# Kernel tuning notes

Hardware: AMD Instinct MI355X
Metric: run time of the kernel (lower is better)

The kernel has to match this reference:

```python
import jax, jax.numpy as jnp
import numpy as np

B, S, F, E, K = 4, 1024, 1024, 8, 2
H = 4 * F  # expert hidden dim, hard-coded as features*4 in the module


def setup_inputs() -> dict:
    key = jax.random.key(0)
    ks = jax.random.split(key, 7)
    def xavier(k, shape):
        fan_in, fan_out = shape[-2], shape[-1]
        scale = jnp.sqrt(6.0 / (fan_in + fan_out))
        return jax.random.uniform(k, shape, jnp.float32, -scale, scale)
    return {
        "x": jax.random.normal(ks[0], (B, S, F), jnp.float32),
        "Wg": xavier(ks[1], (F, E)),
        "bg": jnp.zeros((E,), jnp.float32),
        "W1": xavier(ks[2], (E, F, H)),
        "b1": jnp.zeros((E, H), jnp.float32),
        "W2": xavier(ks[3], (E, H, F)),
        "b2": jnp.zeros((E, F), jnp.float32),
    }


def reference(x, Wg, bg, W1, b1, W2, b2):
    # Gating: softmax over experts, keep top-k, renormalize.
    gate_probs = jax.nn.softmax(x @ Wg + bg, axis=-1)              # (b,s,E)
    k = K
    _, top_idx = jax.lax.top_k(gate_probs, k)                       # (b,s,k)
    expert_mask = jax.nn.one_hot(top_idx, gate_probs.shape[-1],
                                 dtype=gate_probs.dtype).sum(-2)    # (b,s,E)
    selected = gate_probs * expert_mask
    selected = selected / (selected.sum(-1, keepdims=True) + 1e-8)
    # Dense all-expert 2-layer MLP (gelu, tanh approximation as in flax nn.gelu).
    h = jax.nn.gelu(jnp.einsum('bsf,efh->bseh', x, W1) + b1)        # (b,s,E,H)
    expert_out = jnp.einsum('bseh,ehf->bsef', h, W2) + b2[None, None]  # (b,s,E,F)
    # Weighted combine over experts with renormalized top-k gates.
    return jnp.einsum('bsef,bse->bsf', expert_out, selected)
```

## Files before the change

kernel.cpp:

```cpp
#include <hip/hip_runtime.h>
#include <hip/hip_bf16.h>

constexpr int Ff = 1024;
constexpr int Ee = 8;
constexpr int Hh = 4096;
constexpr int T  = 4096;
constexpr int MB = 80;

typedef short     bf16x8 __attribute__((ext_vector_type(8)));
typedef float     f32x4  __attribute__((ext_vector_type(4)));
typedef unsigned short u16x8 __attribute__((ext_vector_type(8)));

__device__ __forceinline__ float gelu_fast(float v) {
  const float c2 = 2.0f * 0.7978845608028654f;
  float z2 = c2 * (v + 0.044715f * v * v * v);
  return v / (1.0f + __expf(-z2));
}

__device__ __forceinline__ unsigned short bf16bits(float f) {
  __hip_bfloat16 h = __float2bfloat16(f);
  return *reinterpret_cast<unsigned short*>(&h);
}

__device__ __forceinline__ void gl_lds16(const void* g, void* l) {
  __builtin_amdgcn_global_load_lds(
      (const __attribute__((address_space(1))) unsigned int*)g,
      (__attribute__((address_space(3))) unsigned int*)l, 16, 0, 0);
}

__global__ __launch_bounds__(256) void gating_kernel(
    const float* __restrict__ x, const float* __restrict__ Wg,
    const float* __restrict__ bg, int* __restrict__ cnt,
    int* __restrict__ list, float* __restrict__ wlist) {
  const int wave = threadIdx.x >> 6;
  const int lane = threadIdx.x & 63;
  const int t = blockIdx.x * 4 + wave;
  float acc[Ee] = {0.f,0.f,0.f,0.f,0.f,0.f,0.f,0.f};
  const float* xrow = x + (size_t)t * Ff;
  for (int f0 = 0; f0 < Ff; f0 += 64) {
    float xv = xrow[f0 + lane];
    const float* wrow = Wg + (size_t)(f0 + lane) * Ee;
    float4 w0 = *reinterpret_cast<const float4*>(wrow);
    float4 w1 = *reinterpret_cast<const float4*>(wrow + 4);
    acc[0] += xv * w0.x; acc[1] += xv * w0.y;
    acc[2] += xv * w0.z; acc[3] += xv * w0.w;
    acc[4] += xv * w1.x; acc[5] += xv * w1.y;
    acc[6] += xv * w1.z; acc[7] += xv * w1.w;
  }
#pragma unroll
  for (int e = 0; e < Ee; ++e) {
#pragma unroll
    for (int off = 32; off; off >>= 1) acc[e] += __shfl_xor(acc[e], off);
  }
  if (lane == 0) {
    float l[Ee], m = -1e30f;
#pragma unroll
    for (int e = 0; e < Ee; ++e) { l[e] = acc[e] + bg[e]; m = fmaxf(m, l[e]); }
    float p[Ee], Z = 0.f;
#pragma unroll
    for (int e = 0; e < Ee; ++e) { p[e] = expf(l[e] - m); Z += p[e]; }
#pragma unroll
    for (int e = 0; e < Ee; ++e) p[e] /= Z;
    int i1 = 0; float p1 = p[0];
#pragma unroll
    for (int e = 1; e < Ee; ++e) if (p[e] > p1) { p1 = p[e]; i1 = e; }
    int i2 = -1; float p2 = -1e30f;
#pragma unroll
    for (int e = 0; e < Ee; ++e) if (e != i1 && p[e] > p2) { p2 = p[e]; i2 = e; }
    float denom = p1 + p2 + 1e-8f;
    int pos = atomicAdd(&cnt[i1], 1);
    list[i1 * T + pos] = t; wlist[i1 * T + pos] = p1 / denom;
    pos = atomicAdd(&cnt[i2], 1);
    list[i2 * T + pos] = t; wlist[i2 * T + pos] = p2 / denom;
  }
}

__global__ void prefix_kernel(const int* __restrict__ cnt, int* __restrict__ offs) {
  if (threadIdx.x == 0) {
    int s = 0;
    for (int e = 0; e < Ee; ++e) { offs[e] = s; s += (cnt[e] + 127) & ~127; }
    offs[Ee] = s;
  }
}

__global__ __launch_bounds__(256) void pack_w_kernel(
    const float* __restrict__ src, unsigned short* __restrict__ dst,
    int sN, size_t s_estride, size_t d_estride, int KT) {
  const int e  = blockIdx.z;
  const int nb = blockIdx.x;
  const int kt = blockIdx.y;
  __shared__ float Ts[128][33];
  const int t = threadIdx.x;
  const float* sb = src + (size_t)e * s_estride + (size_t)(kt * 32) * sN + nb * 128;
  {
    const int row = t >> 5;
    const int cc  = (t & 31) * 4;
#pragma unroll
    for (int i = 0; i < 4; ++i) {
      float4 v = *reinterpret_cast<const float4*>(sb + (size_t)(row + 8 * i) * sN + cc);
      Ts[cc + 0][row + 8 * i] = v.x;
      Ts[cc + 1][row + 8 * i] = v.y;
      Ts[cc + 2][row + 8 * i] = v.z;
      Ts[cc + 3][row + 8 * i] = v.w;
    }
  }
  __syncthreads();
  unsigned short* db = dst + (size_t)e * d_estride + ((size_t)nb * KT + kt) * 4096;
#pragma unroll
  for (int j = 0; j < 2; ++j) {
    const int idx = t + 256 * j;
    const int col = idx & 127, kb = idx >> 7;
    u16x8 o;
#pragma unroll
    for (int q = 0; q < 8; ++q) o[q] = bf16bits(Ts[col][kb * 8 + q]);
    *reinterpret_cast<u16x8*>(db + kb * 1024 + col * 8) = o;
  }
}

__global__ __launch_bounds__(256) void pack_x_kernel(
    const float* __restrict__ x, const int* __restrict__ cnt,
    const int* __restrict__ offs, const int* __restrict__ list,
    unsigned short* __restrict__ xg) {
  const int kt = blockIdx.x;
  const int mb = blockIdx.y;
  const int t = threadIdx.x;
  const int m0g = mb * 128;
  int e = 0;
#pragma unroll
  for (int i = 1; i < Ee; ++i) e += (m0g >= offs[i]) ? 1 : 0;
  const int ce = cnt[e];
  const int row = t >> 1, half = t & 1;
  const int mloc = m0g - offs[e] + row;
  const bool valid = (mloc >= 0) && (mloc < ce);
  const int token = valid ? list[e * T + mloc] : 0;
  const float* sp = x + (size_t)token * Ff + kt * 32 + half * 16;
  u16x8 o0, o1;
#pragma unroll
  for (int i = 0; i < 2; ++i) {
    float4 v = valid ? *reinterpret_cast<const float4*>(sp + i * 4)
                     : make_float4(0.f, 0.f, 0.f, 0.f);
    o0[i * 4 + 0] = bf16bits(v.x); o0[i * 4 + 1] = bf16bits(v.y);
    o0[i * 4 + 2] = bf16bits(v.z); o0[i * 4 + 3] = bf16bits(v.w);
  }
#pragma unroll
  for (int i = 2; i < 4; ++i) {
    float4 v = valid ? *reinterpret_cast<const float4*>(sp + i * 4)
                     : make_float4(0.f, 0.f, 0.f, 0.f);
    o1[(i - 2) * 4 + 0] = bf16bits(v.x); o1[(i - 2) * 4 + 1] = bf16bits(v.y);
    o1[(i - 2) * 4 + 2] = bf16bits(v.z); o1[(i - 2) * 4 + 3] = bf16bits(v.w);
  }
  unsigned short* db = xg + ((size_t)mb * (Ff / 32) + kt) * 4096 + row * 8;
  *reinterpret_cast<u16x8*>(db + (half * 2 + 0) * 1024) = o0;
  *reinterpret_cast<u16x8*>(db + (half * 2 + 1) * 1024) = o1;
}

__global__ __launch_bounds__(256, 3) void gemm1_mfma(
    const unsigned short* __restrict__ xg, const unsigned short* __restrict__ W1P,
    const float* __restrict__ b1, const int* __restrict__ cnt,
    const int* __restrict__ offs, unsigned short* __restrict__ hp, int Hc, int c) {
  const int nxg = Hc >> 7;
  const int nwg = nxg * MB;
  const int raw = blockIdx.x;
  int bid = (raw & 7) * (nwg >> 3) + (raw >> 3);
  const int bw = (nxg >= 4) ? 4 : nxg;
  const int band = bid / (MB * bw);
  const int r2 = bid % (MB * bw);
  const int by = r2 / bw;
  const int bx = band * bw + (r2 % bw);

  const int m0g = by * 128;
  int e = 0;
#pragma unroll
  for (int i = 1; i < Ee; ++i) e += (m0g >= offs[i]) ? 1 : 0;
  const int ce = cnt[e];
  const int mloc = m0g - offs[e];
  if (mloc >= ce) return;
  const int n0 = bx * 128;

  __shared__ __align__(16) unsigned short AsF[3 * 4096];
  __shared__ __align__(16) unsigned short BsF[3 * 4096];

  const int tid = threadIdx.x;
  const int w = tid >> 6, lane = tid & 63;
  const int g = lane >> 4, r16 = lane & 15;
  const int wr = w >> 1, wc = w & 1;

  constexpr int NT = Ff / 32;
  const unsigned short* aU = xg  + (size_t)by * NT * 4096;
  const unsigned short* bU = W1P + (size_t)(e * nxg + bx) * NT * 4096;

  f32x4 acc[4][4] = {};
  auto STAGE = [&](int buf, int kt) {
    const unsigned short* aS = aU + (size_t)kt * 4096 + w * 1024 + lane * 8;
    const unsigned short* bS = bU + (size_t)kt * 4096 + w * 1024 + lane * 8;
    unsigned short* aD = AsF + buf * 4096 + w * 1024;
    unsigned short* bD = BsF + buf * 4096 + w * 1024;
    gl_lds16(aS,       aD);
    gl_lds16(aS + 512, aD + 512);
    gl_lds16(bS,       bD);
    gl_lds16(bS + 512, bD + 512);
  };
  STAGE(0, 0); STAGE(1, 1);
  int cur = 0;
#pragma unroll 1
  for (int t = 0; t < NT; ++t) {
    if (t + 1 < NT) asm volatile("s_waitcnt vmcnt(4)" ::: "memory");
    else            asm volatile("s_waitcnt vmcnt(0)" ::: "memory");
    __builtin_amdgcn_s_barrier();
    asm volatile("" ::: "memory");
    if (t + 2 < NT) STAGE((t + 2) % 3, t + 2);
    bf16x8 af[4], bfr[4];
#pragma unroll
    for (int i = 0; i < 4; ++i) {
      af[i]  = *reinterpret_cast<const bf16x8*>(
          AsF + cur * 4096 + g * 1024 + (wr * 64 + i * 16 + r16) * 8);
      bfr[i] = *reinterpret_cast<const bf16x8*>(
          BsF + cur * 4096 + g * 1024 + (wc * 64 + i * 16 + r16) * 8);
    }
    asm volatile("s_waitcnt lgkmcnt(0)" ::: "memory");
    __builtin_amdgcn_sched_barrier(0);
    __builtin_amdgcn_s_setprio(1);
#pragma unroll
    for (int mi = 0; mi < 4; ++mi)
#pragma unroll
      for (int ni = 0; ni < 4; ++ni)
        acc[mi][ni] = __builtin_amdgcn_mfma_f32_16x16x32_bf16(
            af[mi], bfr[ni], acc[mi][ni], 0, 0, 0);
    __builtin_amdgcn_s_setprio(0);
    asm volatile("" ::: "memory");
    cur = (cur == 2) ? 0 : cur + 1;
  }
  const int KT2 = Hc >> 5;
  unsigned short* hb = hp + (size_t)by * KT2 * 4096;
#pragma unroll
  for (int ni = 0; ni < 4; ++ni) {
    const int col = n0 + wc * 64 + ni * 16 + r16;
    const float bias = b1[(size_t)e * Hh + (size_t)c * Hc + col];
    unsigned short* hcol = hb + ((size_t)(col >> 5) * 4 + ((col >> 3) & 3)) * 1024 + (col & 7);
#pragma unroll
    for (int mi = 0; mi < 4; ++mi)
#pragma unroll
      for (int r = 0; r < 4; ++r) {
        const int row = wr * 64 + mi * 16 + g * 4 + r;
        if (mloc + row < ce)
          hcol[row * 8] = bf16bits(gelu_fast(acc[mi][ni][r] + bias));
      }
  }
}

__global__ __launch_bounds__(256, 3) void gemm2_mfma(
    const unsigned short* __restrict__ hp, const unsigned short* __restrict__ W2P,
    const float* __restrict__ b2, const int* __restrict__ cnt,
    const int* __restrict__ offs, const int* __restrict__ list,
    const float* __restrict__ wlist, float* __restrict__ out,
    int Hc, int kLen, int ksplit, int biasC) {
  constexpr int nxg = Ff >> 7;
  const int nwg = nxg * MB * ksplit;
  const int raw = blockIdx.x;
  int bid = (raw & 7) * (nwg >> 3) + (raw >> 3);
  const int bx = bid % nxg;
  const int rest = bid / nxg;
  const int by = rest % MB;
  const int bz = rest / MB;

  const int m0g = by * 128;
  int e = 0;
#pragma unroll
  for (int i = 1; i < Ee; ++i) e += (m0g >= offs[i]) ? 1 : 0;
  const int ce = cnt[e];
  const int mloc = m0g - offs[e];
  if (mloc >= ce) return;
  const int n0 = bx * 128;

  __shared__ __align__(16) unsigned short AsF[3 * 4096];
  __shared__ __align__(16) unsigned short BsF[3 * 4096];

  const int tid = threadIdx.x;
  const int w = tid >> 6, lane = tid & 63;
  const int g = lane >> 4, r16 = lane & 15;
  const int wr = w >> 1, wc = w & 1;

  const int KT2 = Hc >> 5;
  const int ktOff = (bz * kLen) >> 5;
  const int NT = kLen >> 5;
  const unsigned short* aU = hp  + ((size_t)by * KT2 + ktOff) * 4096;
  const unsigned short* bU = W2P + ((size_t)(e * nxg + bx) * KT2 + ktOff) * 4096;

  f32x4 acc[4][4] = {};
  auto STAGE = [&](int buf, int kt) {
    const unsigned short* aS = aU + (size_t)kt * 4096 + w * 1024 + lane * 8;
    const unsigned short* bS = bU + (size_t)kt * 4096 + w * 1024 + lane * 8;
    unsigned short* aD = AsF + buf * 4096 + w * 1024;
    unsigned short* bD = BsF + buf * 4096 + w * 1024;
    gl_lds16(aS,       aD);
    gl_lds16(aS + 512, aD + 512);
    gl_lds16(bS,       bD);
    gl_lds16(bS + 512, bD + 512);
  };
  STAGE(0, 0);
  if (NT > 1) STAGE(1, 1);
  int cur = 0;
#pragma unroll 1
  for (int t = 0; t < NT; ++t) {
    if (t + 1 < NT) asm volatile("s_waitcnt vmcnt(4)" ::: "memory");
    else            asm volatile("s_waitcnt vmcnt(0)" ::: "memory");
    __builtin_amdgcn_s_barrier();
    asm volatile("" ::: "memory");
    if (t + 2 < NT) STAGE((t + 2) % 3, t + 2);
    bf16x8 af[4], bfr[4];
#pragma unroll
    for (int i = 0; i < 4; ++i) {
      af[i]  = *reinterpret_cast<const bf16x8*>(
          AsF + cur * 4096 + g * 1024 + (wr * 64 + i * 16 + r16) * 8);
      bfr[i] = *reinterpret_cast<const bf16x8*>(
          BsF + cur * 4096 + g * 1024 + (wc * 64 + i * 16 + r16) * 8);
    }
    asm volatile("s_waitcnt lgkmcnt(0)" ::: "memory");
    __builtin_amdgcn_sched_barrier(0);
    __builtin_amdgcn_s_setprio(1);
#pragma unroll
    for (int mi = 0; mi < 4; ++mi)
#pragma unroll
      for (int ni = 0; ni < 4; ++ni)
        acc[mi][ni] = __builtin_amdgcn_mfma_f32_16x16x32_bf16(
            af[mi], bfr[ni], acc[mi][ni], 0, 0, 0);
    __builtin_amdgcn_s_setprio(0);
    asm volatile("" ::: "memory");
    cur = (cur == 2) ? 0 : cur + 1;
  }
  const bool addBias = (biasC != 0) && (bz == 0);
#pragma unroll
  for (int mi = 0; mi < 4; ++mi)
#pragma unroll
    for (int r = 0; r < 4; ++r) {
      const int row = wr * 64 + mi * 16 + g * 4 + r;
      if (mloc + row >= ce) continue;
      const int token = list[e * T + mloc + row];
      const float wgt = wlist[e * T + mloc + row];
      float* op = out + (size_t)token * Ff;
#pragma unroll
      for (int ni = 0; ni < 4; ++ni) {
        const int col = n0 + wc * 64 + ni * 16 + r16;
        float v = acc[mi][ni][r];
        if (addBias) v += b2[(size_t)e * Ff + col];
        atomicAdd(&op[col], wgt * v);
      }
    }
}

extern "C" void kernel_launch(void* const* d_in, const int* in_sizes, int n_in,
                              void* d_out, int out_size, void* d_ws, size_t ws_size,
                              hipStream_t stream) {
  const float* x  = (const float*)d_in[0];
  const float* Wg = (const float*)d_in[1];
  const float* bg = (const float*)d_in[2];
  const float* W1 = (const float*)d_in[3];
  const float* b1 = (const float*)d_in[4];
  const float* W2 = (const float*)d_in[5];
  const float* b2 = (const float*)d_in[6];
  float* out = (float*)d_out;

  const size_t fixed = 1024 + 2 * (size_t)T * Ee * 4 + (size_t)MB * 128 * Ff * 2;
  int Hc = 4096;
  while (Hc > 256 && fixed + (size_t)Hc * 53248 > ws_size) Hc >>= 1;
  const int nchunk = Hh / Hc;
  const int ksplit = 2;
  const int kLen = Hc / ksplit;

  char* p = (char*)d_ws;
  int*   cnt   = (int*)p;            p += 512;
  int*   offs  = (int*)p;            p += 512;
  int*   list  = (int*)p;            p += (size_t)T * Ee * 4;
  float* wlist = (float*)p;          p += (size_t)T * Ee * 4;
  unsigned short* xg  = (unsigned short*)p;  p += (size_t)MB * 128 * Ff * 2;
  unsigned short* W1P = (unsigned short*)p;  p += (size_t)Ee * Hc * Ff * 2;
  unsigned short* W2P = (unsigned short*)p;  p += (size_t)Ee * Ff * Hc * 2;
  unsigned short* hp  = (unsigned short*)p;

  hipMemsetAsync(d_out, 0, (size_t)out_size * sizeof(float), stream);
  hipMemsetAsync(cnt, 0, 64, stream);

  gating_kernel<<<T / 4, 256, 0, stream>>>(x, Wg, bg, cnt, list, wlist);
  prefix_kernel<<<1, 64, 0, stream>>>(cnt, offs);
  pack_x_kernel<<<dim3(Ff / 32, MB), 256, 0, stream>>>(x, cnt, offs, list, xg);

  for (int c = 0; c < nchunk; ++c) {
    pack_w_kernel<<<dim3(Hc / 128, Ff / 32, Ee), 256, 0, stream>>>(
        W1 + (size_t)c * Hc, W1P, Hh, (size_t)Ff * Hh, (size_t)Hc * Ff, Ff / 32);
    pack_w_kernel<<<dim3(Ff / 128, Hc / 32, Ee), 256, 0, stream>>>(
        W2 + (size_t)c * Hc * Ff, W2P, Ff, (size_t)Hh * Ff, (size_t)Ff * Hc, Hc / 32);
    gemm1_mfma<<<(Hc / 128) * MB, 256, 0, stream>>>(
        xg, W1P, b1, cnt, offs, hp, Hc, c);
    gemm2_mfma<<<(Ff / 128) * MB * ksplit, 256, 0, stream>>>(
        hp, W2P, b2, cnt, offs, list, wlist, out, Hc, kLen, ksplit,
        c == nchunk - 1 ? 1 : 0);
  }
}
```

Measured before the change: 501.1 us.

## Enlarge MoE GEMM tiles to 256x128 with 512 threads and K=64 stages

```diff
diff --git a/kernel.cpp b/kernel.cpp
--- a/kernel.cpp
+++ b/kernel.cpp
@@ -5,7 +5,8 @@
 constexpr int Ee = 8;
 constexpr int Hh = 4096;
 constexpr int T  = 4096;
-constexpr int MB = 80;
+constexpr int MB128 = 80;
+constexpr int MBLK  = 40;
 
 typedef short     bf16x8 __attribute__((ext_vector_type(8)));
 typedef float     f32x4  __attribute__((ext_vector_type(4)));
@@ -78,7 +79,7 @@
 __global__ void prefix_kernel(const int* __restrict__ cnt, int* __restrict__ offs) {
   if (threadIdx.x == 0) {
     int s = 0;
-    for (int e = 0; e < Ee; ++e) { offs[e] = s; s += (cnt[e] + 127) & ~127; }
+    for (int e = 0; e < Ee; ++e) { offs[e] = s; s += (cnt[e] + 255) & ~255; }
     offs[Ee] = s;
   }
 }
@@ -154,21 +155,87 @@
   *reinterpret_cast<u16x8*>(db + (half * 2 + 1) * 1024) = o1;
 }
 
-__global__ __launch_bounds__(256, 3) void gemm1_mfma(
+
+#define GEMM_CORE_LOOP(aU0, aU1, bU)                                                    \
+  f32x4 acc[4][4] = {};                                                                 \
+  auto LOAD1 = [&](int l, int tb, int tt) {                                             \
+    const int rgn = l >> 4, j = l & 15;                                                 \
+    const int s2 = j >> 3, kb = (j >> 1) & 3, hh = j & 1;                               \
+    const int off = (s2 * 4 + kb) * 1024 + hh * 512;                                    \
+    unsigned short* dst = (rgn < 2) ? (SMEM + tb * 24576 + rgn * 8192 + off)            \
+                                    : (SMEM + tb * 24576 + 16384 + off);                \
+    const unsigned short* srcb = (rgn == 0) ? (aU0) : (rgn == 1) ? (aU1) : (bU);        \
+    const unsigned short* src = srcb + (size_t)(2 * tt + s2) * 4096 + kb * 1024         \
+                                + hh * 512 + lane * 8;                                  \
+    gl_lds16(src, dst);                                                                 \
+  };                                                                                    \
+  {                                                                                     \
+    for (int i = 0; i < 6; ++i) LOAD1(6 * w + i, 0, 0);                                 \
+    if (NT > 1) { for (int i = 0; i < 6; ++i) LOAD1(6 * w + i, 1, 1); }                 \
+    asm volatile("s_waitcnt vmcnt(6)" ::: "memory");                                    \
+    __builtin_amdgcn_s_barrier();                                                       \
+  }                                                                                     \
+  _Pragma("unroll 1")                                                                   \
+  for (int t = 0; t < NT; ++t) {                                                        \
+    const int cb = t % 3;                                                               \
+    const int tb = (t + 2) % 3;                                                         \
+    const bool st = (t + 2) < NT;                                                       \
+    _Pragma("unroll")                                                                   \
+    for (int ph = 0; ph < 2; ++ph) {                                                    \
+      bf16x8 a2[2][2], b4[4][2];                                                        \
+      _Pragma("unroll")                                                                 \
+      for (int f = 0; f < 2; ++f)                                                       \
+        _Pragma("unroll")                                                               \
+        for (int s = 0; s < 2; ++s) {                                                   \
+          const int row = (wm & 1) * 64 + (ph * 2 + f) * 16 + r16;                      \
+          a2[f][s] = *reinterpret_cast<const bf16x8*>(                                  \
+              SMEM + cb * 24576 + (wm >> 1) * 8192 + (s * 4 + g) * 1024 + row * 8);     \
+        }                                                                               \
+      _Pragma("unroll")                                                                 \
+      for (int nf = 0; nf < 4; ++nf)                                                    \
+        _Pragma("unroll")                                                               \
+        for (int s = 0; s < 2; ++s)                                                     \
+          b4[nf][s] = *reinterpret_cast<const bf16x8*>(                                 \
+              SMEM + cb * 24576 + 16384 + (s * 4 + g) * 1024 +                          \
+              (wn * 64 + nf * 16 + r16) * 8);                                           \
+      if (st) {                                                                         \
+        LOAD1(6 * w + 3 * ph + 0, tb, t + 2);                                           \
+        LOAD1(6 * w + 3 * ph + 1, tb, t + 2);                                           \
+        LOAD1(6 * w + 3 * ph + 2, tb, t + 2);                                           \
+      }                                                                                 \
+      if (ph == 1) {                                                                    \
+        if (st) asm volatile("s_waitcnt vmcnt(6)" ::: "memory");                        \
+        else    asm volatile("s_waitcnt vmcnt(0)" ::: "memory");                        \
+      }                                                                                 \
+      __builtin_amdgcn_s_barrier();                                                     \
+      asm volatile("s_waitcnt lgkmcnt(0)" ::: "memory");                                \
+      __builtin_amdgcn_sched_barrier(0);                                                \
+      __builtin_amdgcn_s_setprio(1);                                                    \
+      _Pragma("unroll")                                                                 \
+      for (int f = 0; f < 2; ++f)                                                       \
+        _Pragma("unroll")                                                               \
+        for (int nf = 0; nf < 4; ++nf)                                                  \
+          _Pragma("unroll")                                                             \
+          for (int s = 0; s < 2; ++s)                                                   \
+            acc[ph * 2 + f][nf] = __builtin_amdgcn_mfma_f32_16x16x32_bf16(              \
+                a2[f][s], b4[nf][s], acc[ph * 2 + f][nf], 0, 0, 0);                     \
+      __builtin_amdgcn_s_setprio(0);                                                    \
+      asm volatile("" ::: "memory");                                                    \
+      __builtin_amdgcn_s_barrier();                                                     \
+    }                                                                                   \
+  }
+
+__global__ __launch_bounds__(512, 2) void gemm1_mfma(
     const unsigned short* __restrict__ xg, const unsigned short* __restrict__ W1P,
     const float* __restrict__ b1, const int* __restrict__ cnt,
     const int* __restrict__ offs, unsigned short* __restrict__ hp, int Hc, int c) {
   const int nxg = Hc >> 7;
-  const int nwg = nxg * MB;
+  const int nwg = nxg * MBLK;
   const int raw = blockIdx.x;
   int bid = (raw & 7) * (nwg >> 3) + (raw >> 3);
-  const int bw = (nxg >= 4) ? 4 : nxg;
-  const int band = bid / (MB * bw);
-  const int r2 = bid % (MB * bw);
-  const int by = r2 / bw;
-  const int bx = band * bw + (r2 % bw);
-
-  const int m0g = by * 128;
+  const int by = bid % MBLK;
+  const int bx = bid / MBLK;
+  const int m0g = by * 256;
   int e = 0;
 #pragma unroll
   for (int i = 1; i < Ee; ++i) e += (m0g >= offs[i]) ? 1 : 0;
@@ -177,93 +244,65 @@
   if (mloc >= ce) return;
   const int n0 = bx * 128;
 
-  __shared__ __align__(16) unsigned short AsF[3 * 4096];
-  __shared__ __align__(16) unsigned short BsF[3 * 4096];
+  __shared__ __align__(16) unsigned short SMEM[73728];
 
   const int tid = threadIdx.x;
   const int w = tid >> 6, lane = tid & 63;
   const int g = lane >> 4, r16 = lane & 15;
-  const int wr = w >> 1, wc = w & 1;
-
-  constexpr int NT = Ff / 32;
-  const unsigned short* aU = xg  + (size_t)by * NT * 4096;
-  const unsigned short* bU = W1P + (size_t)(e * nxg + bx) * NT * 4096;
-
-  f32x4 acc[4][4] = {};
-  auto STAGE = [&](int buf, int kt) {
-    const unsigned short* aS = aU + (size_t)kt * 4096 + w * 1024 + lane * 8;
-    const unsigned short* bS = bU + (size_t)kt * 4096 + w * 1024 + lane * 8;
-    unsigned short* aD = AsF + buf * 4096 + w * 1024;
-    unsigned short* bD = BsF + buf * 4096 + w * 1024;
-    gl_lds16(aS,       aD);
-    gl_lds16(aS + 512, aD + 512);
-    gl_lds16(bS,       bD);
-    gl_lds16(bS + 512, bD + 512);
-  };
-  STAGE(0, 0); STAGE(1, 1);
-  int cur = 0;
-#pragma unroll 1
-  for (int t = 0; t < NT; ++t) {
-    if (t + 1 < NT) asm volatile("s_waitcnt vmcnt(4)" ::: "memory");
-    else            asm volatile("s_waitcnt vmcnt(0)" ::: "memory");
-    __builtin_amdgcn_s_barrier();
-    asm volatile("" ::: "memory");
-    if (t + 2 < NT) STAGE((t + 2) % 3, t + 2);
-    bf16x8 af[4], bfr[4];
-#pragma unroll
-    for (int i = 0; i < 4; ++i) {
-      af[i]  = *reinterpret_cast<const bf16x8*>(
-          AsF + cur * 4096 + g * 1024 + (wr * 64 + i * 16 + r16) * 8);
-      bfr[i] = *reinterpret_cast<const bf16x8*>(
-          BsF + cur * 4096 + g * 1024 + (wc * 64 + i * 16 + r16) * 8);
-    }
-    asm volatile("s_waitcnt lgkmcnt(0)" ::: "memory");
-    __builtin_amdgcn_sched_barrier(0);
-    __builtin_amdgcn_s_setprio(1);
-#pragma unroll
-    for (int mi = 0; mi < 4; ++mi)
-#pragma unroll
-      for (int ni = 0; ni < 4; ++ni)
-        acc[mi][ni] = __builtin_amdgcn_mfma_f32_16x16x32_bf16(
-            af[mi], bfr[ni], acc[mi][ni], 0, 0, 0);
-    __builtin_amdgcn_s_setprio(0);
-    asm volatile("" ::: "memory");
-    cur = (cur == 2) ? 0 : cur + 1;
-  }
+  const int wm = w >> 1, wn = w & 1;
+
+  constexpr int NT = Ff / 64;
+  const unsigned short* aU0 = xg + (size_t)(2 * by + 0) * (Ff / 32) * 4096;
+  const unsigned short* aU1 = xg + (size_t)(2 * by + 1) * (Ff / 32) * 4096;
+  const unsigned short* bU  = W1P + (size_t)(e * nxg + bx) * (Ff / 32) * 4096;
+
+  GEMM_CORE_LOOP(aU0, aU1, bU)
+
+  __builtin_amdgcn_s_barrier();
+  unsigned short* Ls = SMEM;
+#pragma unroll
+  for (int nf = 0; nf < 4; ++nf) {
+    const int col = wn * 64 + nf * 16 + r16;
+    const float bias = b1[(size_t)e * Hh + (size_t)c * Hc + n0 + col];
+#pragma unroll
+    for (int mf = 0; mf < 4; ++mf)
+#pragma unroll
+      for (int r = 0; r < 4; ++r) {
+        const int row = wm * 64 + mf * 16 + g * 4 + r;
+        Ls[row * 136 + col] = bf16bits(gelu_fast(acc[mf][nf][r] + bias));
+      }
+  }
+  __builtin_amdgcn_s_barrier();
   const int KT2 = Hc >> 5;
-  unsigned short* hb = hp + (size_t)by * KT2 * 4096;
-#pragma unroll
-  for (int ni = 0; ni < 4; ++ni) {
-    const int col = n0 + wc * 64 + ni * 16 + r16;
-    const float bias = b1[(size_t)e * Hh + (size_t)c * Hc + col];
-    unsigned short* hcol = hb + ((size_t)(col >> 5) * 4 + ((col >> 3) & 3)) * 1024 + (col & 7);
-#pragma unroll
-    for (int mi = 0; mi < 4; ++mi)
-#pragma unroll
-      for (int r = 0; r < 4; ++r) {
-        const int row = wr * 64 + mi * 16 + g * 4 + r;
-        if (mloc + row < ce)
-          hcol[row * 8] = bf16bits(gelu_fast(acc[mi][ni][r] + bias));
-      }
-  }
-}
-
-__global__ __launch_bounds__(256, 3) void gemm2_mfma(
+#pragma unroll
+  for (int p = 0; p < 8; ++p) {
+    const int u = p * 512 + tid;
+    const int oct = u >> 8;
+    const int row = u & 255;
+    const int lc = oct * 8;
+    unsigned short* dst = hp +
+        ((size_t)(2 * by + (row >> 7)) * KT2 + ((n0 + lc) >> 5)) * 4096 +
+        ((lc >> 3) & 3) * 1024 + (row & 127) * 8;
+    *reinterpret_cast<u16x8*>(dst) = *reinterpret_cast<const u16x8*>(&Ls[row * 136 + lc]);
+  }
+}
+
+__global__ __launch_bounds__(512, 2) void gemm2_mfma(
     const unsigned short* __restrict__ hp, const unsigned short* __restrict__ W2P,
     const float* __restrict__ b2, const int* __restrict__ cnt,
     const int* __restrict__ offs, const int* __restrict__ list,
     const float* __restrict__ wlist, float* __restrict__ out,
     int Hc, int kLen, int ksplit, int biasC) {
   constexpr int nxg = Ff >> 7;
-  const int nwg = nxg * MB * ksplit;
+  const int nwg = nxg * MBLK * ksplit;
   const int raw = blockIdx.x;
   int bid = (raw & 7) * (nwg >> 3) + (raw >> 3);
   const int bx = bid % nxg;
   const int rest = bid / nxg;
-  const int by = rest % MB;
-  const int bz = rest / MB;
-
-  const int m0g = by * 128;
+  const int by = rest % MBLK;
+  const int bz = rest / MBLK;
+
+  const int m0g = by * 256;
   int e = 0;
 #pragma unroll
   for (int i = 1; i < Ee; ++i) e += (m0g >= offs[i]) ? 1 : 0;
@@ -272,76 +311,36 @@
   if (mloc >= ce) return;
   const int n0 = bx * 128;
 
-  __shared__ __align__(16) unsigned short AsF[3 * 4096];
-  __shared__ __align__(16) unsigned short BsF[3 * 4096];
+  __shared__ __align__(16) unsigned short SMEM[73728];
 
   const int tid = threadIdx.x;
   const int w = tid >> 6, lane = tid & 63;
   const int g = lane >> 4, r16 = lane & 15;
-  const int wr = w >> 1, wc = w & 1;
+  const int wm = w >> 1, wn = w & 1;
 
   const int KT2 = Hc >> 5;
   const int ktOff = (bz * kLen) >> 5;
-  const int NT = kLen >> 5;
-  const unsigned short* aU = hp  + ((size_t)by * KT2 + ktOff) * 4096;
-  const unsigned short* bU = W2P + ((size_t)(e * nxg + bx) * KT2 + ktOff) * 4096;
-
-  f32x4 acc[4][4] = {};
-  auto STAGE = [&](int buf, int kt) {
-    const unsigned short* aS = aU + (size_t)kt * 4096 + w * 1024 + lane * 8;
-    const unsigned short* bS = bU + (size_t)kt * 4096 + w * 1024 + lane * 8;
-    unsigned short* aD = AsF + buf * 4096 + w * 1024;
-    unsigned short* bD = BsF + buf * 4096 + w * 1024;
-    gl_lds16(aS,       aD);
-    gl_lds16(aS + 512, aD + 512);
-    gl_lds16(bS,       bD);
-    gl_lds16(bS + 512, bD + 512);
-  };
-  STAGE(0, 0);
-  if (NT > 1) STAGE(1, 1);
-  int cur = 0;
-#pragma unroll 1
-  for (int t = 0; t < NT; ++t) {
-    if (t + 1 < NT) asm volatile("s_waitcnt vmcnt(4)" ::: "memory");
-    else            asm volatile("s_waitcnt vmcnt(0)" ::: "memory");
-    __builtin_amdgcn_s_barrier();
-    asm volatile("" ::: "memory");
-    if (t + 2 < NT) STAGE((t + 2) % 3, t + 2);
-    bf16x8 af[4], bfr[4];
-#pragma unroll
-    for (int i = 0; i < 4; ++i) {
-      af[i]  = *reinterpret_cast<const bf16x8*>(
-          AsF + cur * 4096 + g * 1024 + (wr * 64 + i * 16 + r16) * 8);
-      bfr[i] = *reinterpret_cast<const bf16x8*>(
-          BsF + cur * 4096 + g * 1024 + (wc * 64 + i * 16 + r16) * 8);
-    }
-    asm volatile("s_waitcnt lgkmcnt(0)" ::: "memory");
-    __builtin_amdgcn_sched_barrier(0);
-    __builtin_amdgcn_s_setprio(1);
-#pragma unroll
-    for (int mi = 0; mi < 4; ++mi)
-#pragma unroll
-      for (int ni = 0; ni < 4; ++ni)
-        acc[mi][ni] = __builtin_amdgcn_mfma_f32_16x16x32_bf16(
-            af[mi], bfr[ni], acc[mi][ni], 0, 0, 0);
-    __builtin_amdgcn_s_setprio(0);
-    asm volatile("" ::: "memory");
-    cur = (cur == 2) ? 0 : cur + 1;
-  }
+  const int NT = kLen >> 6;
+  const unsigned short* aU0 = hp + ((size_t)(2 * by + 0) * KT2 + ktOff) * 4096;
+  const unsigned short* aU1 = hp + ((size_t)(2 * by + 1) * KT2 + ktOff) * 4096;
+  const unsigned short* bU  = W2P + ((size_t)(e * nxg + bx) * KT2 + ktOff) * 4096;
+
+  GEMM_CORE_LOOP(aU0, aU1, bU)
+
   const bool addBias = (biasC != 0) && (bz == 0);
 #pragma unroll
-  for (int mi = 0; mi < 4; ++mi)
+  for (int mf = 0; mf < 4; ++mf)
 #pragma unroll
     for (int r = 0; r < 4; ++r) {
-      const int row = wr * 64 + mi * 16 + g * 4 + r;
+      const int row = wm * 64 + mf * 16 + g * 4 + r;
       if (mloc + row >= ce) continue;
       const int token = list[e * T + mloc + row];
       const float wgt = wlist[e * T + mloc + row];
       float* op = out + (size_t)token * Ff;
 #pragma unroll
-      for (int ni = 0; ni < 4; ++ni) {
-        const int col = n0 + wc * 64 + ni * 16 + r16;
-        float v = acc[mi][ni][r];
+      for (int nf = 0; nf < 4; ++nf) {
+        const int col = n0 + wn * 64 + nf * 16 + r16;
+        float v = acc[mf][nf][r];
         if (addBias) v += b2[(size_t)e * Ff + col];
         atomicAdd(&op[col], wgt * v);
       }
@@ -360,7 +359,7 @@
   const float* b2 = (const float*)d_in[6];
   float* out = (float*)d_out;
 
-  const size_t fixed = 1024 + 2 * (size_t)T * Ee * 4 + (size_t)MB * 128 * Ff * 2;
+  const size_t fixed = 1024 + 2 * (size_t)T * Ee * 4 + (size_t)MB128 * 128 * Ff * 2;
   int Hc = 4096;
   while (Hc > 256 && fixed + (size_t)Hc * 53248 > ws_size) Hc >>= 1;
   const int nchunk = Hh / Hc;
@@ -372,7 +371,7 @@
   int*   offs  = (int*)p;            p += 512;
   int*   list  = (int*)p;            p += (size_t)T * Ee * 4;
   float* wlist = (float*)p;          p += (size_t)T * Ee * 4;
-  unsigned short* xg  = (unsigned short*)p;  p += (size_t)MB * 128 * Ff * 2;
+  unsigned short* xg  = (unsigned short*)p;  p += (size_t)MB128 * 128 * Ff * 2;
   unsigned short* W1P = (unsigned short*)p;  p += (size_t)Ee * Hc * Ff * 2;
   unsigned short* W2P = (unsigned short*)p;  p += (size_t)Ee * Ff * Hc * 2;
   unsigned short* hp  = (unsigned short*)p;
@@ -382,16 +381,16 @@
 
   gating_kernel<<<T / 4, 256, 0, stream>>>(x, Wg, bg, cnt, list, wlist);
   prefix_kernel<<<1, 64, 0, stream>>>(cnt, offs);
-  pack_x_kernel<<<dim3(Ff / 32, MB), 256, 0, stream>>>(x, cnt, offs, list, xg);
+  pack_x_kernel<<<dim3(Ff / 32, MB128), 256, 0, stream>>>(x, cnt, offs, list, xg);
 
   for (int c = 0; c < nchunk; ++c) {
     pack_w_kernel<<<dim3(Hc / 128, Ff / 32, Ee), 256, 0, stream>>>(
         W1 + (size_t)c * Hc, W1P, Hh, (size_t)Ff * Hh, (size_t)Hc * Ff, Ff / 32);
     pack_w_kernel<<<dim3(Ff / 128, Hc / 32, Ee), 256, 0, stream>>>(
         W2 + (size_t)c * Hc * Ff, W2P, Ff, (size_t)Hh * Ff, (size_t)Ff * Hc, Hc / 32);
-    gemm1_mfma<<<(Hc / 128) * MB, 256, 0, stream>>>(
+    gemm1_mfma<<<(Hc / 128) * MBLK, 512, 0, stream>>>(
         xg, W1P, b1, cnt, offs, hp, Hc, c);
-    gemm2_mfma<<<(Ff / 128) * MB * ksplit, 256, 0, stream>>>(
+    gemm2_mfma<<<(Ff / 128) * MBLK * ksplit, 512, 0, stream>>>(
         hp, W2P, b2, cnt, offs, list, wlist, out, Hc, kLen, ksplit,
         c == nchunk - 1 ? 1 : 0);
   }
```

Result: slower. 511.3 us (+2.0%).
